# Performance work log

Hardware: AMD Instinct MI355X
Metric: run time of the kernel (lower is better)

Reference implementation:

```python
import jax, jax.numpy as jnp
import numpy as np

N, C, H, W = 4, 128, 28, 28
K, D = 64, 512  # num_clusters, dim_center
EPS = 1e-12     # torch F.normalize eps


def setup_inputs() -> dict:
    key = jax.random.key(0)
    k1, k2, k3, k4 = jax.random.split(key, 4)
    x = jax.random.normal(k1, (N, C, H, W), dtype=jnp.float32)
    # 1x1 conv weight (dim_center, dim) with kaiming-normal fan_out scale, bias zero
    conv_w = jax.random.normal(k2, (D, C), dtype=jnp.float32) * np.float32(np.sqrt(2.0 / D))
    conv_b = jnp.zeros((D,), dtype=jnp.float32)
    # centroids initialized with torch.rand -> uniform [0,1)
    centroids = jax.random.uniform(k3, (K, D), dtype=jnp.float32)
    return {"x": x, "conv_w": conv_w, "conv_b": conv_b, "centroids": centroids}


def reference(x, conv_w, conv_b, centroids):
    n, c, h, w = x.shape
    # descriptor-wise L2 normalization over channel dim (torch F.normalize, p=2, dim=1)
    nrm = jnp.sqrt(jnp.sum(x * x, axis=1, keepdims=True))
    xn = x / jnp.maximum(nrm, EPS)
    # 1x1 conv == per-pixel matmul: (N,C,H,W) x (D,C) -> (N,D,H,W)
    feat = jnp.einsum('nchw,dc->ndhw', xn, conv_w) + conv_b[None, :, None, None]
    xf = feat.reshape(n, D, h * w)  # (N, D, P)
    # residual[n,k,d,p] = xf[n,d,p] - centroids[k,d]
    resid = xf[:, None, :, :] - centroids[None, :, :, None]  # (N, K, D, P)
    soft_assign = jax.nn.softmax(resid, axis=-1)             # softmax over spatial P
    vlad = jnp.sum(soft_assign * xf[:, None, :, :], axis=-1)  # (N, K, D)
    return vlad
```

## Files before the change

### kernel.cpp

```cpp
#include <hip/hip_runtime.h>
#include <math.h>

#define NB 4
#define CC 128
#define HW 784
#define KK 64
#define DD 512
#define TD 8
#define PXB 392
#define CH 64
#define BLK 832

__global__ __launch_bounds__(BLK, 7) void netvlad_gemm_partial(
    const float* __restrict__ x, const float* __restrict__ w,
    const float* __restrict__ b, float2* __restrict__ pws)
{
    __shared__ float w_s[CC][TD];
    __shared__ float feat_s[TD][PXB];
    __shared__ float sq_s[PXB];

    const int tid = threadIdx.x;
    const int bb  = blockIdx.x;
    const int n   = bb >> 7;
    const int dg  = (bb >> 1) & 63;
    const int h   = bb & 1;
    const int d0  = dg * TD;
    const int p0  = h * PXB;

    for (int i = tid; i < CC * TD; i += BLK) {
        int c = i >> 3, j = i & 7;
        w_s[c][j] = w[(size_t)(d0 + j) * CC + c];
    }

    const int  ch    = (tid >= 416) ? 1 : 0;
    const int  praw  = tid - ch * 416;
    const bool act   = praw < PXB;
    const int  p_loc = act ? praw : 0;
    const int  cb    = ch * CH;

    __syncthreads();

    const float* xp = x + (size_t)n * CC * HW + (size_t)cb * HW + (p0 + p_loc);

    float acc[TD];
    #pragma unroll
    for (int j = 0; j < TD; ++j) acc[j] = 0.f;
    float sq = 0.f;

    #pragma unroll 8
    for (int c = 0; c < CH; ++c) {
        float xv = xp[(size_t)c * HW];
        float4 wlo = *(const float4*)&w_s[cb + c][0];
        float4 whi = *(const float4*)&w_s[cb + c][4];
        sq = fmaf(xv, xv, sq);
        acc[0] = fmaf(wlo.x, xv, acc[0]);
        acc[1] = fmaf(wlo.y, xv, acc[1]);
        acc[2] = fmaf(wlo.z, xv, acc[2]);
        acc[3] = fmaf(wlo.w, xv, acc[3]);
        acc[4] = fmaf(whi.x, xv, acc[4]);
        acc[5] = fmaf(whi.y, xv, acc[5]);
        acc[6] = fmaf(whi.z, xv, acc[6]);
        acc[7] = fmaf(whi.w, xv, acc[7]);
    }

    if (act && ch == 0) {
        sq_s[p_loc] = sq;
        #pragma unroll
        for (int j = 0; j < TD; ++j) feat_s[j][p_loc] = acc[j];
    }
    __syncthreads();
    if (act && ch == 1) {
        float r = 1.0f / fmaxf(sqrtf(sq_s[p_loc] + sq), 1e-12f);
        #pragma unroll
        for (int j = 0; j < TD; ++j)
            feat_s[j][p_loc] = fmaf(feat_s[j][p_loc] + acc[j], r, b[d0 + j]);
    }
    __syncthreads();

    const int lane = tid & 63;
    const int wave = tid >> 6;
    if (wave < TD) {
        const int j = wave;
        float s = 0.f, ws = 0.f;
        for (int q = lane; q < PXB; q += 64) {
            float f = feat_s[j][q];
            float e = __expf(f);
            s += e;
            ws = fmaf(e, f, ws);
        }
        #pragma unroll
        for (int off = 32; off; off >>= 1) {
            s  += __shfl_xor(s, off, 64);
            ws += __shfl_xor(ws, off, 64);
        }
        if (lane == 0)
            pws[(size_t)(n * DD + d0 + j) * 2 + h] = make_float2(s, ws);
    }
}

__global__ __launch_bounds__(512) void netvlad_finalize(
    const float2* __restrict__ pws, float* __restrict__ out)
{
    const int d  = threadIdx.x;
    const int n  = blockIdx.x >> 3;
    const int ks = (blockIdx.x & 7) * 8;
    float2 a = pws[(size_t)(n * DD + d) * 2 + 0];
    float2 c = pws[(size_t)(n * DD + d) * 2 + 1];
    float g = (a.y + c.y) / (a.x + c.x);
    #pragma unroll
    for (int i = 0; i < 8; ++i)
        out[(size_t)n * KK * DD + (size_t)(ks + i) * DD + d] = g;
}

extern "C" void kernel_launch(void* const* d_in, const int* in_sizes, int n_in,
                              void* d_out, int out_size, void* d_ws, size_t ws_size,
                              hipStream_t stream) {
    const float* x = (const float*)d_in[0];
    const float* w = (const float*)d_in[1];
    const float* b = (const float*)d_in[2];
    float2* pws = (float2*)d_ws;
    float* out  = (float*)d_out;

    netvlad_gemm_partial<<<NB * (DD / TD) * 2, BLK, 0, stream>>>(x, w, b, pws);
    netvlad_finalize<<<32, 512, 0, stream>>>(pws, out);
}
```

Baseline: 19.47 us.

## Double per-block output channels and remap blocks for XCD-local x reuse

Each block now computes 16 output channels instead of 8. This halves the grid and the number of times each x column is re-read from global memory. Block indices are remapped so that blocks sharing the same batch image land on the same XCD, which should improve L2 reuse of x. The channel loop also batches eight x loads before the FMAs to expose memory-level parallelism. The costs are more registers per thread, a dropped occupancy hint, and fewer blocks (256), so latency hiding and CU coverage may suffer.

```diff
diff --git a/kernel.cpp b/kernel.cpp
--- a/kernel.cpp
+++ b/kernel.cpp
@@ -6,36 +6,39 @@
 #define HW 784
 #define KK 64
 #define DD 512
-#define TD 8
+#define TD 16
 #define PXB 392
 #define CH 64
+#define HTH 416
 #define BLK 832
 
-__global__ __launch_bounds__(BLK, 7) void netvlad_gemm_partial(
+__global__ __launch_bounds__(BLK) void netvlad_gemm_partial(
     const float* __restrict__ x, const float* __restrict__ w,
     const float* __restrict__ b, float2* __restrict__ pws)
 {
     __shared__ float w_s[CC][TD];
-    __shared__ float feat_s[TD][PXB];
+    __shared__ float acc_s[TD][PXB];
     __shared__ float sq_s[PXB];
 
-    const int tid = threadIdx.x;
-    const int bb  = blockIdx.x;
-    const int n   = bb >> 7;
-    const int dg  = (bb >> 1) & 63;
-    const int h   = bb & 1;
-    const int d0  = dg * TD;
-    const int p0  = h * PXB;
+    const int tid  = threadIdx.x;
+    const int bid  = blockIdx.x;
+    const int xcd  = bid & 7;
+    const int slot = bid >> 3;
+    const int n    = xcd >> 1;
+    const int dg   = ((slot >> 1) << 1) | (xcd & 1);
+    const int h    = slot & 1;
+    const int d0   = dg * TD;
+    const int p0   = h * PXB;
 
     for (int i = tid; i < CC * TD; i += BLK) {
-        int c = i >> 3, j = i & 7;
+        int c = i >> 4, j = i & 15;
         w_s[c][j] = w[(size_t)(d0 + j) * CC + c];
     }
 
-    const int  ch    = (tid >= 416) ? 1 : 0;
-    const int  praw  = tid - ch * 416;
-    const bool act   = praw < PXB;
-    const int  p_loc = act ? praw : 0;
+    const int  ch    = (tid >= HTH) ? 1 : 0;
+    const int  qr    = tid - ch * HTH;
+    const bool act   = qr < PXB;
+    const int  p_loc = act ? qr : 0;
     const int  cb    = ch * CH;
 
     __syncthreads();
@@ -47,54 +50,74 @@
     for (int j = 0; j < TD; ++j) acc[j] = 0.f;
     float sq = 0.f;
 
-    #pragma unroll 8
-    for (int c = 0; c < CH; ++c) {
-        float xv = xp[(size_t)c * HW];
-        float4 wlo = *(const float4*)&w_s[cb + c][0];
-        float4 whi = *(const float4*)&w_s[cb + c][4];
-        sq = fmaf(xv, xv, sq);
-        acc[0] = fmaf(wlo.x, xv, acc[0]);
-        acc[1] = fmaf(wlo.y, xv, acc[1]);
-        acc[2] = fmaf(wlo.z, xv, acc[2]);
-        acc[3] = fmaf(wlo.w, xv, acc[3]);
-        acc[4] = fmaf(whi.x, xv, acc[4]);
-        acc[5] = fmaf(whi.y, xv, acc[5]);
-        acc[6] = fmaf(whi.z, xv, acc[6]);
-        acc[7] = fmaf(whi.w, xv, acc[7]);
+    for (int cc = 0; cc < CH; cc += 8) {
+        float xv[8];
+        #pragma unroll
+        for (int u = 0; u < 8; ++u)
+            xv[u] = xp[(size_t)(cc + u) * HW];
+        #pragma unroll
+        for (int u = 0; u < 8; ++u) {
+            const int c = cb + cc + u;
+            float4 w0 = *(const float4*)&w_s[c][0];
+            float4 w1 = *(const float4*)&w_s[c][4];
+            float4 w2 = *(const float4*)&w_s[c][8];
+            float4 w3 = *(const float4*)&w_s[c][12];
+            float xvu = xv[u];
+            sq = fmaf(xvu, xvu, sq);
+            acc[0]  = fmaf(w0.x, xvu, acc[0]);
+            acc[1]  = fmaf(w0.y, xvu, acc[1]);
+            acc[2]  = fmaf(w0.z, xvu, acc[2]);
+            acc[3]  = fmaf(w0.w, xvu, acc[3]);
+            acc[4]  = fmaf(w1.x, xvu, acc[4]);
+            acc[5]  = fmaf(w1.y, xvu, acc[5]);
+            acc[6]  = fmaf(w1.z, xvu, acc[6]);
+            acc[7]  = fmaf(w1.w, xvu, acc[7]);
+            acc[8]  = fmaf(w2.x, xvu, acc[8]);
+            acc[9]  = fmaf(w2.y, xvu, acc[9]);
+            acc[10] = fmaf(w2.z, xvu, acc[10]);
+            acc[11] = fmaf(w2.w, xvu, acc[11]);
+            acc[12] = fmaf(w3.x, xvu, acc[12]);
+            acc[13] = fmaf(w3.y, xvu, acc[13]);
+            acc[14] = fmaf(w3.z, xvu, acc[14]);
+            acc[15] = fmaf(w3.w, xvu, acc[15]);
+        }
     }
 
     if (act && ch == 0) {
         sq_s[p_loc] = sq;
         #pragma unroll
-        for (int j = 0; j < TD; ++j) feat_s[j][p_loc] = acc[j];
+        for (int j = 0; j < TD; ++j) acc_s[j][p_loc] = acc[j];
     }
     __syncthreads();
     if (act && ch == 1) {
         float r = 1.0f / fmaxf(sqrtf(sq_s[p_loc] + sq), 1e-12f);
         #pragma unroll
         for (int j = 0; j < TD; ++j)
-            feat_s[j][p_loc] = fmaf(feat_s[j][p_loc] + acc[j], r, b[d0 + j]);
+            acc_s[j][p_loc] = fmaf(acc_s[j][p_loc] + acc[j], r, b[d0 + j]);
     }
     __syncthreads();
 
     const int lane = tid & 63;
     const int wave = tid >> 6;
-    if (wave < TD) {
-        const int j = wave;
-        float s = 0.f, ws = 0.f;
-        for (int q = lane; q < PXB; q += 64) {
-            float f = feat_s[j][q];
-            float e = __expf(f);
-            s += e;
-            ws = fmaf(e, f, ws);
+    if (wave < 8) {
+        #pragma unroll
+        for (int rr = 0; rr < 2; ++rr) {
+            const int j = wave * 2 + rr;
+            float s = 0.f, ws = 0.f;
+            for (int q = lane; q < PXB; q += 64) {
+                float f = acc_s[j][q];
+                float e = __expf(f);
+                s += e;
+                ws = fmaf(e, f, ws);
+            }
+            #pragma unroll
+            for (int off = 32; off; off >>= 1) {
+                s  += __shfl_xor(s, off, 64);
+                ws += __shfl_xor(ws, off, 64);
+            }
+            if (lane == 0)
+                pws[(size_t)(n * DD + d0 + j) * 2 + h] = make_float2(s, ws);
         }
-        #pragma unroll
-        for (int off = 32; off; off >>= 1) {
-            s  += __shfl_xor(s, off, 64);
-            ws += __shfl_xor(ws, off, 64);
-        }
-        if (lane == 0)
-            pws[(size_t)(n * DD + d0 + j) * 2 + h] = make_float2(s, ws);
     }
 }
 
```

Result: no change. 19.19 us (-1.5%).
